# Optimization experiments

Hardware: AMD Instinct MI355X
Metric: run time of the kernel (lower is better)

The kernel has to match this reference:

```python
import jax, jax.numpy as jnp
import numpy as np

B, NH, T, D = 2, 16, 2048, 64

def setup_inputs() -> dict:
    key = jax.random.key(0)
    kq, kk, kv = jax.random.split(key, 3)
    Q = jax.random.normal(kq, (B, NH, T, D), dtype=jnp.float32)
    K = jax.random.normal(kk, (B, NH, T, D), dtype=jnp.float32)
    V = jax.random.normal(kv, (B, NH, T, D), dtype=jnp.float32)
    return {"Q": Q, "K": K, "V": V}

def reference(Q, K, V):
    # scores: [B, nh, T, T]
    Dh = Q.shape[-1]
    scale = 1.0 / jnp.sqrt(jnp.asarray(Dh, Q.dtype))
    scores = jnp.einsum('bhtd,bhsd->bhts', Q, K) * scale
    Tq = Q.shape[2]
    causal = jnp.tril(jnp.ones((Tq, Tq), dtype=bool))
    scores = jnp.where(causal, scores, jnp.asarray(-jnp.inf, scores.dtype))
    attn = jax.nn.softmax(scores, axis=-1)
    return jnp.einsum('bhts,bhsd->bhtd', attn, V)
```

## Files before the change

kernel.cpp:

```cpp
#include <hip/hip_runtime.h>
#include <hip/hip_bf16.h>


typedef __bf16 bf16;
typedef __bf16 bf16x4 __attribute__((ext_vector_type(4)));
typedef __bf16 bf16x8 __attribute__((ext_vector_type(8)));
typedef float floatx4 __attribute__((ext_vector_type(4)));

#define T_SEQ 2048
#define DH 64
#define TQ 128
#define TKS 32
#define BHN 32
#define CEXP 0.18033688011112042f

__device__ __forceinline__ void gload16(const bf16* g, bf16* l) {
    __builtin_amdgcn_global_load_lds(
        (const __attribute__((address_space(1))) void*)g,
        (__attribute__((address_space(3))) void*)l, 16, 0, 0);
}

__global__ __launch_bounds__(256) void prep(const float* __restrict__ K,
                                            const float* __restrict__ V,
                                            bf16* __restrict__ Kb,
                                            bf16* __restrict__ Vt) {
    const int bid = (int)blockIdx.x;
    const int tid = (int)threadIdx.x;
    if (bid < 512) {
        size_t i = ((size_t)bid * 256 + tid) * 8;
        #pragma unroll
        for (int it = 0; it < 4; ++it) {
            float4 a = *(const float4*)(K + i + 0);
            float4 b = *(const float4*)(K + i + 4);
            bf16x8 o;
            o[0]=(bf16)a.x; o[1]=(bf16)a.y; o[2]=(bf16)a.z; o[3]=(bf16)a.w;
            o[4]=(bf16)b.x; o[5]=(bf16)b.y; o[6]=(bf16)b.z; o[7]=(bf16)b.w;
            *(bf16x8*)(Kb + i) = o;
            i += (size_t)512 * 256 * 8;
        }
        return;
    }
    __shared__ bf16 tile[2][64][72];
    const int vb = bid - 512;
    const int bh = vb & (BHN - 1);
    const int tp = (vb >> 5) * 128;
    #pragma unroll
    for (int tt = 0; tt < 2; ++tt) {
        const int r = tid >> 2;
        const int c = (tid & 3) * 16;
        const float* s = V + ((size_t)bh * T_SEQ + tp + tt * 64 + r) * DH + c;
        float4 f0 = *(const float4*)(s + 0);
        float4 f1 = *(const float4*)(s + 4);
        float4 f2 = *(const float4*)(s + 8);
        float4 f3 = *(const float4*)(s + 12);
        bf16x8 p0, p1;
        p0[0]=(bf16)f0.x; p0[1]=(bf16)f0.y; p0[2]=(bf16)f0.z; p0[3]=(bf16)f0.w;
        p0[4]=(bf16)f1.x; p0[5]=(bf16)f1.y; p0[6]=(bf16)f1.z; p0[7]=(bf16)f1.w;
        p1[0]=(bf16)f2.x; p1[1]=(bf16)f2.y; p1[2]=(bf16)f2.z; p1[3]=(bf16)f2.w;
        p1[4]=(bf16)f3.x; p1[5]=(bf16)f3.y; p1[6]=(bf16)f3.z; p1[7]=(bf16)f3.w;
        *(bf16x8*)&tile[tt][r][c + 0] = p0;
        *(bf16x8*)&tile[tt][r][c + 8] = p1;
    }
    __syncthreads();
    #pragma unroll
    for (int tt = 0; tt < 2; ++tt) {
        const int d   = tid >> 2;
        const int tch = (tid & 3) * 16;
        bf16x8 o0, o1;
        #pragma unroll
        for (int j = 0; j < 8; ++j) { o0[j] = tile[tt][tch + j][d]; o1[j] = tile[tt][tch + 8 + j][d]; }
        bf16* o = Vt + ((size_t)bh * DH + d) * T_SEQ + tp + tt * 64 + tch;
        *(bf16x8*)(o + 0) = o0;
        *(bf16x8*)(o + 8) = o1;
    }
}

__global__ __launch_bounds__(512, 4)
void fa_fwd(const float* __restrict__ Qg, const bf16* __restrict__ Kb,
            const bf16* __restrict__ Vt, float* __restrict__ Og)
{
    __shared__ __align__(16) bf16 smem[26624];

    const int gid  = (int)blockIdx.x;
    const int half = gid >> 8;
    const int idx  = gid & 255;
    const int bh   = idx & (BHN - 1);
    const int p_   = idx >> 5;
    const int iq   = half ? p_ : (15 - p_);
    const int q0   = iq * TQ;
    const int nsteps = 2 * iq + 2;

    const int tid  = (int)threadIdx.x;
    const int wave = tid >> 6;
    const int w4   = wave & 3;
    const int grp  = wave >> 2;
    const int lane = tid & 63;
    const int quad = lane >> 4;
    const int l16  = lane & 15;

    bf16* Kbuf0 = smem + (grp * 2 + 0) * 2048;
    bf16* Kbuf1 = smem + (grp * 2 + 1) * 2048;
    bf16* Vbuf0 = smem + 8192 + (grp * 2 + 0) * 2048;
    bf16* Vbuf1 = smem + 8192 + (grp * 2 + 1) * 2048;
    bf16* Pw    = smem + 16384 + wave * 1280;

    const bf16* Kbh = Kb + (size_t)bh * (T_SEQ * DH);
    const bf16* Vbh = Vt + (size_t)bh * (DH * T_SEQ);
    const size_t qrb = (size_t)bh * T_SEQ;
    const int qw = q0 + w4 * 32;

    const int krow = w4 * 8  + (lane >> 3);
    const int kgch = (lane & 7) ^ ((lane >> 3) & 7);
    const int vrow = w4 * 16 + (lane >> 2);
    const int vgch = (lane & 3) ^ ((lane >> 3) & 3);

    bf16x8 qb[2][2];
    #pragma unroll
    for (int nt = 0; nt < 2; ++nt) {
        const int qrow = qw + nt * 16 + l16;
        #pragma unroll
        for (int kk = 0; kk < 2; ++kk) {
            const float* s = Qg + (qrb + qrow) * DH + kk * 32 + quad * 8;
            float4 f0 = *(const float4*)(s);
            float4 f1 = *(const float4*)(s + 4);
            bf16x8 t;
            t[0]=(bf16)f0.x; t[1]=(bf16)f0.y; t[2]=(bf16)f0.z; t[3]=(bf16)f0.w;
            t[4]=(bf16)f1.x; t[5]=(bf16)f1.y; t[6]=(bf16)f1.z; t[7]=(bf16)f1.w;
            qb[nt][kk] = t;
        }
    }

    floatx4 oacc[4][2];
    #pragma unroll
    for (int mt = 0; mt < 4; ++mt)
        #pragma unroll
        for (int nt = 0; nt < 2; ++nt) oacc[mt][nt] = (floatx4){0.f,0.f,0.f,0.f};
    float lpart[2] = {0.f, 0.f};

    auto stage = [&](int kt, bf16* kb, bf16* vb) {
        const int k0 = kt * TKS;
        gload16(Kbh + (size_t)(k0 + krow) * DH + kgch * 8, kb + w4 * 512);
        gload16(Vbh + (size_t)vrow * T_SEQ + k0 + vgch * 8, vb + w4 * 512);
    };

    stage(grp, Kbuf0, Vbuf0);
    __syncthreads();

    for (int s = 0; s < nsteps; ++s) {
        const int cur = s & 1;
        if (s + 1 < nsteps)
            stage(2 * (s + 1) + grp, cur ? Kbuf0 : Kbuf1, cur ? Vbuf0 : Vbuf1);

        const int kt = 2 * s + grp;
        const int k0 = kt * TKS;
        const bf16* Kcur = cur ? Kbuf1 : Kbuf0;
        const bf16* Vcur = cur ? Vbuf1 : Vbuf0;

        if (k0 <= qw + 31) {
            floatx4 sa[2][2];
            #pragma unroll
            for (int mt = 0; mt < 2; ++mt)
                #pragma unroll
                for (int nt = 0; nt < 2; ++nt) sa[mt][nt] = (floatx4){0.f,0.f,0.f,0.f};
            #pragma unroll
            for (int kk = 0; kk < 2; ++kk) {
                #pragma unroll
                for (int mt = 0; mt < 2; ++mt) {
                    bf16x8 kf = *(const bf16x8*)&Kcur[(mt * 16 + l16) * 64 + (((kk * 4 + quad) ^ (l16 & 7)) * 8)];
                    sa[mt][0] = __builtin_amdgcn_mfma_f32_16x16x32_bf16(kf, qb[0][kk], sa[mt][0], 0, 0, 0);
                    sa[mt][1] = __builtin_amdgcn_mfma_f32_16x16x32_bf16(kf, qb[1][kk], sa[mt][1], 0, 0, 0);
                }
            }
            if (k0 + TKS - 1 > qw) {
                #pragma unroll
                for (int mt = 0; mt < 2; ++mt)
                    #pragma unroll
                    for (int nt = 0; nt < 2; ++nt) {
                        const int qg = qw + nt * 16 + l16;
                        #pragma unroll
                        for (int r = 0; r < 4; ++r) {
                            const int keyg = k0 + mt * 16 + quad * 4 + r;
                            if (keyg > qg) sa[mt][nt][r] = -INFINITY;
                        }
                    }
            }
            #pragma unroll
            for (int mt = 0; mt < 2; ++mt)
                #pragma unroll
                for (int nt = 0; nt < 2; ++nt) {
                    bf16x4 w;
                    #pragma unroll
                    for (int r = 0; r < 4; ++r) {
                        const float pv = __builtin_amdgcn_exp2f(CEXP * sa[mt][nt][r]);
                        lpart[nt] += pv;
                        w[r] = (bf16)pv;
                    }
                    *(bf16x4*)&Pw[(nt * 16 + l16) * 40 + mt * 16 + quad * 4] = w;
                }
            bf16x8 pf[2];
            #pragma unroll
            for (int nt = 0; nt < 2; ++nt)
                pf[nt] = *(const bf16x8*)&Pw[(nt * 16 + l16) * 40 + quad * 8];
            #pragma unroll
            for (int mt = 0; mt < 4; ++mt) {
                bf16x8 vf = *(const bf16x8*)&Vcur[(mt * 16 + l16) * 32 + ((quad ^ ((l16 >> 1) & 3)) * 8)];
                oacc[mt][0] = __builtin_amdgcn_mfma_f32_16x16x32_bf16(vf, pf[0], oacc[mt][0], 0, 0, 0);
                oacc[mt][1] = __builtin_amdgcn_mfma_f32_16x16x32_bf16(vf, pf[1], oacc[mt][1], 0, 0, 0);
            }
        }

        __syncthreads();
    }

    float* cb  = (float*)smem + w4 * 2048;
    float* lbs = (float*)(smem + 16384) + w4 * 128;
    if (grp == 1) {
        #pragma unroll
        for (int mt = 0; mt < 4; ++mt)
            #pragma unroll
            for (int nt = 0; nt < 2; ++nt)
                *(floatx4*)&cb[((mt * 2 + nt) * 64 + lane) * 4] = oacc[mt][nt];
        lbs[lane * 2 + 0] = lpart[0];
        lbs[lane * 2 + 1] = lpart[1];
    }
    __syncthreads();
    if (grp == 0) {
        lpart[0] += lbs[lane * 2 + 0];
        lpart[1] += lbs[lane * 2 + 1];
        float invl[2];
        #pragma unroll
        for (int nt = 0; nt < 2; ++nt) {
            float v = lpart[nt];
            v += __shfl_xor(v, 16);
            v += __shfl_xor(v, 32);
            invl[nt] = 1.0f / v;
        }
        #pragma unroll
        for (int nt = 0; nt < 2; ++nt) {
            const size_t qrow = qrb + qw + nt * 16 + l16;
            #pragma unroll
            for (int mt = 0; mt < 4; ++mt) {
                floatx4 ob = *(const floatx4*)&cb[((mt * 2 + nt) * 64 + lane) * 4];
                float4 o;
                o.x = (oacc[mt][nt][0] + ob[0]) * invl[nt];
                o.y = (oacc[mt][nt][1] + ob[1]) * invl[nt];
                o.z = (oacc[mt][nt][2] + ob[2]) * invl[nt];
                o.w = (oacc[mt][nt][3] + ob[3]) * invl[nt];
                *(float4*)&Og[qrow * DH + mt * 16 + quad * 4] = o;
            }
        }
    }
}

extern "C" void kernel_launch(void* const* d_in, const int* in_sizes, int n_in,
                              void* d_out, int out_size, void* d_ws, size_t ws_size,
                              hipStream_t stream) {
    const float* Q = (const float*)d_in[0];
    const float* K = (const float*)d_in[1];
    const float* V = (const float*)d_in[2];
    float* O = (float*)d_out;
    (void)in_sizes; (void)n_in; (void)out_size; (void)ws_size;

    const size_t nelem = (size_t)BHN * T_SEQ * DH;
    bf16* Kbf = (bf16*)d_ws;
    bf16* Vtb = Kbf + nelem;

    prep<<<dim3(1024), dim3(256), 0, stream>>>(K, V, Kbf, Vtb);
    fa_fwd<<<dim3(512), dim3(512), 0, stream>>>(Q, Kbf, Vtb, O);
}
```

Measured before the change: 122.7 us.

## Pair heavy and light 64-row query blocks per workgroup with split-K waves

Each workgroup now handles two 64-row query blocks, one from the top and one from the bottom of the causal triangle, so every block covers the same 66 key tiles. The four waves split that key range into contiguous chunks and each streams its own K/V through private LDS buffers, which removes the per-step workgroup barrier. When a wave crosses from the heavy block to the light block, it parks its partial output in bf16 registers and reloads Q. Partial outputs and row sums are combined through LDS at the end, rounded to bf16, which costs extra registers and some precision in the reduction.

```diff
diff --git a/kernel.cpp b/kernel.cpp
--- a/kernel.cpp
+++ b/kernel.cpp
@@ -9,7 +9,6 @@
 
 #define T_SEQ 2048
 #define DH 64
-#define TQ 128
 #define TKS 32
 #define BHN 32
 #define CEXP 0.18033688011112042f
@@ -75,177 +74,271 @@
     }
 }
 
-__global__ __launch_bounds__(512, 4)
+__global__ __launch_bounds__(256, 2)
 void fa_fwd(const float* __restrict__ Qg, const bf16* __restrict__ Kb,
             const bf16* __restrict__ Vt, float* __restrict__ Og)
 {
-    __shared__ __align__(16) bf16 smem[26624];
-
-    const int gid  = (int)blockIdx.x;
-    const int half = gid >> 8;
-    const int idx  = gid & 255;
-    const int bh   = idx & (BHN - 1);
-    const int p_   = idx >> 5;
-    const int iq   = half ? p_ : (15 - p_);
-    const int q0   = iq * TQ;
-    const int nsteps = 2 * iq + 2;
+    __shared__ __align__(16) bf16 smem[32768];
+
+    const int gid = (int)blockIdx.x;
+    const int bh  = gid & (BHN - 1);
+    const int m   = gid >> 5;
+    const int B   = 64 - 2 * m;
+    const int qh  = (31 - m) * 64;
+    const int ql  = m * 64;
 
     const int tid  = (int)threadIdx.x;
     const int wave = tid >> 6;
-    const int w4   = wave & 3;
-    const int grp  = wave >> 2;
     const int lane = tid & 63;
     const int quad = lane >> 4;
     const int l16  = lane & 15;
 
-    bf16* Kbuf0 = smem + (grp * 2 + 0) * 2048;
-    bf16* Kbuf1 = smem + (grp * 2 + 1) * 2048;
-    bf16* Vbuf0 = smem + 8192 + (grp * 2 + 0) * 2048;
-    bf16* Vbuf1 = smem + 8192 + (grp * 2 + 1) * 2048;
-    bf16* Pw    = smem + 16384 + wave * 1280;
+    const int tw0 = (wave < 2) ? wave * 17 : 34 + (wave - 2) * 16;
+    const int tw1 = tw0 + ((wave < 2) ? 17 : 16);
+
+    bf16* W   = smem + wave * 8192;
+    bf16* Kb0 = W;
+    bf16* Kb1 = W + 2048;
+    bf16* Vb  = W + 4096;
+    bf16* Pw  = W + 6144;
 
     const bf16* Kbh = Kb + (size_t)bh * (T_SEQ * DH);
     const bf16* Vbh = Vt + (size_t)bh * (DH * T_SEQ);
     const size_t qrb = (size_t)bh * T_SEQ;
-    const int qw = q0 + w4 * 32;
-
-    const int krow = w4 * 8  + (lane >> 3);
-    const int kgch = (lane & 7) ^ ((lane >> 3) & 7);
-    const int vrow = w4 * 16 + (lane >> 2);
-    const int vgch = (lane & 3) ^ ((lane >> 3) & 3);
-
-    bf16x8 qb[2][2];
-    #pragma unroll
-    for (int nt = 0; nt < 2; ++nt) {
-        const int qrow = qw + nt * 16 + l16;
-        #pragma unroll
-        for (int kk = 0; kk < 2; ++kk) {
-            const float* s = Qg + (qrb + qrow) * DH + kk * 32 + quad * 8;
-            float4 f0 = *(const float4*)(s);
-            float4 f1 = *(const float4*)(s + 4);
-            bf16x8 t;
-            t[0]=(bf16)f0.x; t[1]=(bf16)f0.y; t[2]=(bf16)f0.z; t[3]=(bf16)f0.w;
-            t[4]=(bf16)f1.x; t[5]=(bf16)f1.y; t[6]=(bf16)f1.z; t[7]=(bf16)f1.w;
-            qb[nt][kk] = t;
-        }
-    }
-
-    floatx4 oacc[4][2];
+
+    const int rl  = lane >> 3;
+    const int kch = (lane & 7) ^ (rl & 7);
+    const int vr  = lane >> 2;
+    const int vch = (lane & 3) ^ ((lane >> 3) & 3);
+    const int psw = (l16 >> 1) & 3;
+
+    bool heavyNow = (tw0 < B);
+    int  qbase    = heavyNow ? qh : ql;
+
+    bf16x8 qb[4][2];
+    auto loadQ = [&](int qb0) {
+        #pragma unroll
+        for (int nt = 0; nt < 4; ++nt) {
+            const int qrow = qb0 + nt * 16 + l16;
+            #pragma unroll
+            for (int kk = 0; kk < 2; ++kk) {
+                const float* s = Qg + (qrb + qrow) * DH + kk * 32 + quad * 8;
+                float4 f0 = *(const float4*)(s);
+                float4 f1 = *(const float4*)(s + 4);
+                bf16x8 t;
+                t[0]=(bf16)f0.x; t[1]=(bf16)f0.y; t[2]=(bf16)f0.z; t[3]=(bf16)f0.w;
+                t[4]=(bf16)f1.x; t[5]=(bf16)f1.y; t[6]=(bf16)f1.z; t[7]=(bf16)f1.w;
+                qb[nt][kk] = t;
+            }
+        }
+    };
+    loadQ(qbase);
+
+    floatx4 oacc[4][4];
     #pragma unroll
     for (int mt = 0; mt < 4; ++mt)
         #pragma unroll
-        for (int nt = 0; nt < 2; ++nt) oacc[mt][nt] = (floatx4){0.f,0.f,0.f,0.f};
-    float lpart[2] = {0.f, 0.f};
-
-    auto stage = [&](int kt, bf16* kb, bf16* vb) {
+        for (int nt = 0; nt < 4; ++nt) oacc[mt][nt] = (floatx4){0.f,0.f,0.f,0.f};
+    float lpart[4] = {0.f, 0.f, 0.f, 0.f};
+    bf16x4 parked[16];
+    #pragma unroll
+    for (int f = 0; f < 16; ++f) parked[f] = (bf16x4){(bf16)0.f,(bf16)0.f,(bf16)0.f,(bf16)0.f};
+    float lpark[4] = {0.f, 0.f, 0.f, 0.f};
+    bool hasPark = false;
+
+    auto kTileOf = [&](int t) { return (t < B) ? t : (t - B); };
+
+    auto stageK = [&](int kt, bf16* dst) {
+        const bf16* kg = Kbh + (size_t)kt * TKS * DH;
+        #pragma unroll
+        for (int g = 0; g < 4; ++g)
+            gload16(kg + (size_t)(g * 8 + rl) * DH + kch * 8, dst + g * 512);
+    };
+    auto stageV = [&](int kt) {
+        const bf16* vg = Vbh + kt * TKS;
+        #pragma unroll
+        for (int g = 0; g < 4; ++g)
+            gload16(vg + (size_t)(g * 16 + vr) * T_SEQ + vch * 8, Vb + g * 512);
+    };
+
+    stageK(kTileOf(tw0), Kb0);
+
+    for (int t = tw0; t < tw1; ++t) {
+        if (heavyNow && t == B) {
+            #pragma unroll
+            for (int f = 0; f < 16; ++f) {
+                bf16x4 w;
+                #pragma unroll
+                for (int e = 0; e < 4; ++e) w[e] = (bf16)oacc[f >> 2][f & 3][e];
+                parked[f] = w;
+            }
+            #pragma unroll
+            for (int nt = 0; nt < 4; ++nt) { lpark[nt] = lpart[nt]; lpart[nt] = 0.f; }
+            #pragma unroll
+            for (int mt = 0; mt < 4; ++mt)
+                #pragma unroll
+                for (int nt = 0; nt < 4; ++nt) oacc[mt][nt] = (floatx4){0.f,0.f,0.f,0.f};
+            hasPark = true;
+            heavyNow = false;
+            qbase = ql;
+            loadQ(ql);
+        }
+
+        const int cur = (t - tw0) & 1;
+        bf16* Kcur = cur ? Kb1 : Kb0;
+        const int kt = kTileOf(t);
         const int k0 = kt * TKS;
-        gload16(Kbh + (size_t)(k0 + krow) * DH + kgch * 8, kb + w4 * 512);
-        gload16(Vbh + (size_t)vrow * T_SEQ + k0 + vgch * 8, vb + w4 * 512);
-    };
-
-    stage(grp, Kbuf0, Vbuf0);
-    __syncthreads();
-
-    for (int s = 0; s < nsteps; ++s) {
-        const int cur = s & 1;
-        if (s + 1 < nsteps)
-            stage(2 * (s + 1) + grp, cur ? Kbuf0 : Kbuf1, cur ? Vbuf0 : Vbuf1);
-
-        const int kt = 2 * s + grp;
-        const int k0 = kt * TKS;
-        const bf16* Kcur = cur ? Kbuf1 : Kbuf0;
-        const bf16* Vcur = cur ? Vbuf1 : Vbuf0;
-
-        if (k0 <= qw + 31) {
-            floatx4 sa[2][2];
-            #pragma unroll
-            for (int mt = 0; mt < 2; ++mt)
-                #pragma unroll
-                for (int nt = 0; nt < 2; ++nt) sa[mt][nt] = (floatx4){0.f,0.f,0.f,0.f};
+
+        stageV(kt);
+        stageK(kTileOf(t + 1), cur ? Kb0 : Kb1);
+        __builtin_amdgcn_s_waitcnt(0x0F78);
+
+        #pragma unroll
+        for (int mt = 0; mt < 2; ++mt) {
+            floatx4 sa[4];
+            #pragma unroll
+            for (int nt = 0; nt < 4; ++nt) sa[nt] = (floatx4){0.f,0.f,0.f,0.f};
             #pragma unroll
             for (int kk = 0; kk < 2; ++kk) {
-                #pragma unroll
-                for (int mt = 0; mt < 2; ++mt) {
-                    bf16x8 kf = *(const bf16x8*)&Kcur[(mt * 16 + l16) * 64 + (((kk * 4 + quad) ^ (l16 & 7)) * 8)];
-                    sa[mt][0] = __builtin_amdgcn_mfma_f32_16x16x32_bf16(kf, qb[0][kk], sa[mt][0], 0, 0, 0);
-                    sa[mt][1] = __builtin_amdgcn_mfma_f32_16x16x32_bf16(kf, qb[1][kk], sa[mt][1], 0, 0, 0);
-                }
-            }
-            if (k0 + TKS - 1 > qw) {
-                #pragma unroll
-                for (int mt = 0; mt < 2; ++mt)
-                    #pragma unroll
-                    for (int nt = 0; nt < 2; ++nt) {
-                        const int qg = qw + nt * 16 + l16;
-                        #pragma unroll
-                        for (int r = 0; r < 4; ++r) {
-                            const int keyg = k0 + mt * 16 + quad * 4 + r;
-                            if (keyg > qg) sa[mt][nt][r] = -INFINITY;
-                        }
-                    }
-            }
-            #pragma unroll
-            for (int mt = 0; mt < 2; ++mt)
-                #pragma unroll
-                for (int nt = 0; nt < 2; ++nt) {
-                    bf16x4 w;
+                bf16x8 kf = *(const bf16x8*)&Kcur[(mt * 16 + l16) * 64 + (((kk * 4 + quad) ^ (l16 & 7)) * 8)];
+                #pragma unroll
+                for (int nt = 0; nt < 4; ++nt)
+                    sa[nt] = __builtin_amdgcn_mfma_f32_16x16x32_bf16(kf, qb[nt][kk], sa[nt], 0, 0, 0);
+            }
+            if (k0 + TKS - 1 > qbase) {
+                #pragma unroll
+                for (int nt = 0; nt < 4; ++nt) {
+                    const int qg = qbase + nt * 16 + l16;
                     #pragma unroll
                     for (int r = 0; r < 4; ++r) {
-                        const float pv = __builtin_amdgcn_exp2f(CEXP * sa[mt][nt][r]);
-                        lpart[nt] += pv;
-                        w[r] = (bf16)pv;
+                        const int keyg = k0 + mt * 16 + quad * 4 + r;
+                        if (keyg > qg) sa[nt][r] = -INFINITY;
                     }
-                    *(bf16x4*)&Pw[(nt * 16 + l16) * 40 + mt * 16 + quad * 4] = w;
                 }
-            bf16x8 pf[2];
-            #pragma unroll
-            for (int nt = 0; nt < 2; ++nt)
-                pf[nt] = *(const bf16x8*)&Pw[(nt * 16 + l16) * 40 + quad * 8];
-            #pragma unroll
-            for (int mt = 0; mt < 4; ++mt) {
-                bf16x8 vf = *(const bf16x8*)&Vcur[(mt * 16 + l16) * 32 + ((quad ^ ((l16 >> 1) & 3)) * 8)];
-                oacc[mt][0] = __builtin_amdgcn_mfma_f32_16x16x32_bf16(vf, pf[0], oacc[mt][0], 0, 0, 0);
-                oacc[mt][1] = __builtin_amdgcn_mfma_f32_16x16x32_bf16(vf, pf[1], oacc[mt][1], 0, 0, 0);
-            }
-        }
-
-        __syncthreads();
-    }
-
-    float* cb  = (float*)smem + w4 * 2048;
-    float* lbs = (float*)(smem + 16384) + w4 * 128;
-    if (grp == 1) {
-        #pragma unroll
-        for (int mt = 0; mt < 4; ++mt)
-            #pragma unroll
-            for (int nt = 0; nt < 2; ++nt)
-                *(floatx4*)&cb[((mt * 2 + nt) * 64 + lane) * 4] = oacc[mt][nt];
-        lbs[lane * 2 + 0] = lpart[0];
-        lbs[lane * 2 + 1] = lpart[1];
-    }
+            }
+            #pragma unroll
+            for (int nt = 0; nt < 4; ++nt) {
+                bf16x4 w;
+                #pragma unroll
+                for (int r = 0; r < 4; ++r) {
+                    const float pv = __builtin_amdgcn_exp2f(CEXP * sa[nt][r]);
+                    lpart[nt] += pv;
+                    w[r] = (bf16)pv;
+                }
+                const int slot = (mt * 2 + (quad >> 1)) ^ psw;
+                *(bf16x4*)&Pw[(nt * 16 + l16) * 32 + slot * 8 + (quad & 1) * 4] = w;
+            }
+        }
+
+        bf16x8 pf[4];
+        #pragma unroll
+        for (int nt = 0; nt < 4; ++nt)
+            pf[nt] = *(const bf16x8*)&Pw[(nt * 16 + l16) * 32 + ((quad ^ psw) * 8)];
+
+        __builtin_amdgcn_s_waitcnt(0x0F74);
+
+        #pragma unroll
+        for (int mt = 0; mt < 4; ++mt) {
+            bf16x8 vf = *(const bf16x8*)&Vb[(mt * 16 + l16) * 32 + ((quad ^ psw) * 8)];
+            #pragma unroll
+            for (int nt = 0; nt < 4; ++nt)
+                oacc[mt][nt] = __builtin_amdgcn_mfma_f32_16x16x32_bf16(vf, pf[nt], oacc[mt][nt], 0, 0, 0);
+        }
+    }
+
     __syncthreads();
-    if (grp == 0) {
-        lpart[0] += lbs[lane * 2 + 0];
-        lpart[1] += lbs[lane * 2 + 1];
-        float invl[2];
-        #pragma unroll
-        for (int nt = 0; nt < 2; ++nt) {
+    const bool hH = (tw0 < B);
+    const bool hL = (tw1 > B);
+    if (wave >= 1 && hH) {
+        bf16* a = smem + (wave - 1) * 4608;
+        float* al = (float*)(a + 4096);
+        #pragma unroll
+        for (int f = 0; f < 16; ++f) {
+            bf16x4 w;
+            if (hasPark) w = parked[f];
+            else {
+                #pragma unroll
+                for (int e = 0; e < 4; ++e) w[e] = (bf16)oacc[f >> 2][f & 3][e];
+            }
+            *(bf16x4*)&a[(f * 64 + lane) * 4] = w;
+        }
+        #pragma unroll
+        for (int nt = 0; nt < 4; ++nt)
+            al[nt * 64 + lane] = hasPark ? lpark[nt] : lpart[nt];
+    }
+    if (wave >= 2 && hL) {
+        bf16* a = smem + (wave + 1) * 4608;
+        float* al = (float*)(a + 4096);
+        #pragma unroll
+        for (int f = 0; f < 16; ++f) {
+            bf16x4 w;
+            #pragma unroll
+            for (int e = 0; e < 4; ++e) w[e] = (bf16)oacc[f >> 2][f & 3][e];
+            *(bf16x4*)&a[(f * 64 + lane) * 4] = w;
+        }
+        #pragma unroll
+        for (int nt = 0; nt < 4; ++nt)
+            al[nt * 64 + lane] = lpart[nt];
+    }
+    __syncthreads();
+
+    if (wave <= 1) {
+        int qfin;
+        if (wave == 0) {
+            qfin = qh;
+            const int nA = (B > 50) ? 3 : ((B > 34) ? 2 : 1);
+            for (int i = 0; i < nA; ++i) {
+                const bf16* a = smem + i * 4608;
+                const float* al = (const float*)(a + 4096);
+                #pragma unroll
+                for (int f = 0; f < 16; ++f) {
+                    bf16x4 w = *(const bf16x4*)&a[(f * 64 + lane) * 4];
+                    #pragma unroll
+                    for (int e = 0; e < 4; ++e) oacc[f >> 2][f & 3][e] += (float)w[e];
+                }
+                #pragma unroll
+                for (int nt = 0; nt < 4; ++nt) lpart[nt] += al[nt * 64 + lane];
+            }
+        } else {
+            qfin = ql;
+            #pragma unroll
+            for (int mt = 0; mt < 4; ++mt)
+                #pragma unroll
+                for (int nt = 0; nt < 4; ++nt) oacc[mt][nt] = (floatx4){0.f,0.f,0.f,0.f};
+            #pragma unroll
+            for (int nt = 0; nt < 4; ++nt) lpart[nt] = 0.f;
+            const int i0 = (B < 50) ? 3 : 4;
+            for (int i = i0; i <= 4; ++i) {
+                const bf16* a = smem + i * 4608;
+                const float* al = (const float*)(a + 4096);
+                #pragma unroll
+                for (int f = 0; f < 16; ++f) {
+                    bf16x4 w = *(const bf16x4*)&a[(f * 64 + lane) * 4];
+                    #pragma unroll
+                    for (int e = 0; e < 4; ++e) oacc[f >> 2][f & 3][e] += (float)w[e];
+                }
+                #pragma unroll
+                for (int nt = 0; nt < 4; ++nt) lpart[nt] += al[nt * 64 + lane];
+            }
+        }
+        float invl[4];
+        #pragma unroll
+        for (int nt = 0; nt < 4; ++nt) {
             float v = lpart[nt];
             v += __shfl_xor(v, 16);
             v += __shfl_xor(v, 32);
             invl[nt] = 1.0f / v;
         }
         #pragma unroll
-        for (int nt = 0; nt < 2; ++nt) {
-            const size_t qrow = qrb + qw + nt * 16 + l16;
+        for (int nt = 0; nt < 4; ++nt) {
+            const size_t qrow = qrb + qfin + nt * 16 + l16;
             #pragma unroll
             for (int mt = 0; mt < 4; ++mt) {
-                floatx4 ob = *(const floatx4*)&cb[((mt * 2 + nt) * 64 + lane) * 4];
                 float4 o;
-                o.x = (oacc[mt][nt][0] + ob[0]) * invl[nt];
-                o.y = (oacc[mt][nt][1] + ob[1]) * invl[nt];
-                o.z = (oacc[mt][nt][2] + ob[2]) * invl[nt];
-                o.w = (oacc[mt][nt][3] + ob[3]) * invl[nt];
+                o.x = oacc[mt][nt][0] * invl[nt];
+                o.y = oacc[mt][nt][1] * invl[nt];
+                o.z = oacc[mt][nt][2] * invl[nt];
+                o.w = oacc[mt][nt][3] * invl[nt];
                 *(float4*)&Og[qrow * DH + mt * 16 + quad * 4] = o;
             }
         }
@@ -266,5 +359,5 @@
     bf16* Vtb = Kbf + nelem;
 
     prep<<<dim3(1024), dim3(256), 0, stream>>>(K, V, Kbf, Vtb);
-    fa_fwd<<<dim3(512), dim3(512), 0, stream>>>(Q, Kbf, Vtb, O);
+    fa_fwd<<<dim3(512), dim3(256), 0, stream>>>(Q, Kbf, Vtb, O);
 }
```

Result: no change. 124.0 us (+1.0%).
